# Performance work log

Hardware: AMD Instinct MI355X
Metric: run time of the kernel (lower is better)

Reference implementation:

```python
import jax, jax.numpy as jnp
import numpy as np

L = 4096      # number of nodes (treated as sequence length, batch=1)
D = 256       # in_channels == out_channels
H = 8         # heads
DH = D // H   # head dim = 32
NUM_EDGE_TYPES = 14


def setup_inputs() -> dict:
    key = jax.random.key(0)
    ks = jax.random.split(key, 7)
    x = jax.random.normal(ks[0], (L, D), dtype=jnp.float32)
    mask = jax.random.randint(ks[1], (L, L), 0, NUM_EDGE_TYPES, dtype=jnp.int64)
    s = 1.0 / np.sqrt(D)
    in_proj_w = jax.random.uniform(ks[2], (3 * D, D), jnp.float32, -s, s)
    in_proj_b = jnp.zeros((3 * D,), jnp.float32)
    out_proj_w = jax.random.uniform(ks[3], (D, D), jnp.float32, -s, s)
    out_proj_b = jnp.zeros((D,), jnp.float32)
    edge_bias = jax.random.normal(ks[4], (NUM_EDGE_TYPES, H), dtype=jnp.float32) * 0.02
    return {"x": x, "mask": mask, "in_proj_w": in_proj_w, "in_proj_b": in_proj_b,
            "out_proj_w": out_proj_w, "out_proj_b": out_proj_b, "edge_bias": edge_bias}


def reference(x, mask, in_proj_w, in_proj_b, out_proj_w, out_proj_b, edge_bias):
    # x: (L, D) node features -> viewed as batch-1 self-attention, edge-aware scores.
    qkv = x @ in_proj_w.T + in_proj_b                 # (L, 3D)
    q, k, v = jnp.split(qkv, 3, axis=-1)              # each (L, D)
    q = q.reshape(L, H, DH).transpose(1, 0, 2)        # (H, L, DH)
    k = k.reshape(L, H, DH).transpose(1, 0, 2)
    v = v.reshape(L, H, DH).transpose(1, 0, 2)
    scale = 1.0 / jnp.sqrt(jnp.asarray(DH, x.dtype))
    scores = jnp.einsum('hqd,hkd->hqk', q, k) * scale  # (H, L, L)
    # edge-type bias folded into attention scores: lookup (L,L)->(L,L,H)->(H,L,L)
    scores = scores + edge_bias[mask].transpose(2, 0, 1)
    attn = jax.nn.softmax(scores, axis=-1)             # (H, L, L)
    out = jnp.einsum('hqk,hkd->hqd', attn, v)          # (H, L, DH)
    out = out.transpose(1, 0, 2).reshape(L, D)         # merge heads
    return out @ out_proj_w.T + out_proj_b             # (L, D)
```

## Files before the change

kernel.cpp:

```cpp
#include <hip/hip_runtime.h>
#include <hip/hip_bf16.h>
#include <string.h>

#define L 4096
#define D 256
#define H 8
#define DH 32

typedef __attribute__((ext_vector_type(8))) short bf16x8;
typedef __attribute__((ext_vector_type(4))) float f32x4;

#define LOG2E 1.4426950408889634f
#define RS (0.17677669529663688f * LOG2E)

__device__ __forceinline__ ushort f2bf(float f) {
    union { float f; unsigned int i; } v; v.f = f;
    unsigned int x = v.i;
    return (ushort)((x + 0x7fffu + ((x >> 16) & 1u)) >> 16);
}
__device__ __forceinline__ bf16x8 cvt8(const float* p) {
    float4 a = *(const float4*)p;
    float4 b = *(const float4*)(p + 4);
    bf16x8 r;
    r[0] = (short)f2bf(a.x); r[1] = (short)f2bf(a.y);
    r[2] = (short)f2bf(a.z); r[3] = (short)f2bf(a.w);
    r[4] = (short)f2bf(b.x); r[5] = (short)f2bf(b.y);
    r[6] = (short)f2bf(b.z); r[7] = (short)f2bf(b.w);
    return r;
}
__device__ __forceinline__ unsigned int pkbf(float a, float b) {
    float2 t; t.x = a; t.y = b;
    __hip_bfloat162 r = __float22bfloat162_rn(t);
    unsigned int u; memcpy(&u, &r, 4);
    return u;
}
__device__ __forceinline__ float uaf(unsigned int u) {
    union { unsigned int u; float f; } v; v.u = u; return v.f;
}

__device__ __forceinline__ int ksig(int u) {
    return 32 * (u >> 5) + 16 * ((u >> 2) & 1) + 4 * ((u >> 3) & 3) + (u & 3);
}

__global__ __launch_bounds__(256) void pack_kernel(
        const int* __restrict__ mask, const float* __restrict__ x,
        const float* __restrict__ wi, const float* __restrict__ wo,
        unsigned int* __restrict__ m2, ushort* __restrict__ xb,
        ushort* __restrict__ wib, ushort* __restrict__ wob)
{
    const int b = blockIdx.x;
    const int tid = threadIdx.x;
    if (b < 512) {
        __shared__ unsigned int rb[8 * 1025];
        const int4* src = (const int4*)(mask + (size_t)b * 8 * 4096);
#pragma unroll
        for (int i = 0; i < 32; i++) {
            const int g = i * 256 + tid;
            int4 v = src[g];
            rb[(g >> 10) * 1025 + (g & 1023)] =
                ((unsigned int)(v.x & 15) << 4)  | ((unsigned int)(v.y & 15) << 12) |
                ((unsigned int)(v.z & 15) << 20) | ((unsigned int)(v.w & 15) << 28);
        }
        __syncthreads();
        const int t = b >> 1, half = b & 1;
#pragma unroll
        for (int i = 0; i < 32; i++) {
            const int dd = i * 256 + tid;
            const int nt = dd & 3, s = (dd >> 2) & 7, qd = (dd >> 5) & 3, kt = dd >> 7;
            const unsigned int w =
                rb[s * 1025 + kt * 16 + 8 * (nt >> 1) + 2 * qd + (nt & 1)];
            const unsigned int e0 = (w >> 4) & 15u, e1 = (w >> 12) & 15u;
            const unsigned int e2 = (w >> 20) & 15u, e3 = w >> 28;
            const unsigned int p01 = e0 * 14u + e1, p23 = e2 * 14u + e3;
            m2[(size_t)t * 16384 + kt * 256 + (qd * 16 + 8 * half + s) * 4 + nt] =
                (p01 * 68u) | ((p23 * 68u) << 16);
        }
    } else if (b < 1024) {
        const int t = (b - 512) * 256 + tid;
        ((bf16x8*)xb)[t] = cvt8(x + t * 8);
    } else if (b < 1120) {
        const int t = (b - 1024) * 256 + tid;
        ((bf16x8*)wib)[t] = cvt8(wi + t * 8);
    } else {
        const int t = (b - 1120) * 256 + tid;
        ((bf16x8*)wob)[t] = cvt8(wo + t * 8);
    }
}

__global__ __launch_bounds__(256) void qkv_kernel(
        const ushort* __restrict__ xb, const ushort* __restrict__ wb,
        const float* __restrict__ b,
        ushort* __restrict__ Qb, ushort* __restrict__ Kb, ushort* __restrict__ Vt)
{
    const int lane = threadIdx.x & 63, wv = threadIdx.x >> 6;
    const int quad = lane >> 4, l15 = lane & 15;
    const int m0 = blockIdx.x * 64 + wv * 16;
    const int n0 = blockIdx.y * 64;

    f32x4 acc[4] = {};
    for (int ks = 0; ks < 8; ks++) {
        const int kd = ks * 32 + quad * 8;
        bf16x8 af = *(const bf16x8*)(xb + (m0 + l15) * D + kd);
#pragma unroll
        for (int nt = 0; nt < 4; nt++) {
            bf16x8 bfr = *(const bf16x8*)(wb + (n0 + nt * 16 + l15) * D + kd);
            acc[nt] = __builtin_amdgcn_mfma_f32_16x16x32_bf16(af, bfr, acc[nt], 0, 0, 0);
        }
    }
#pragma unroll
    for (int nt = 0; nt < 4; nt++) {
        const int j = n0 + nt * 16 + l15;
        const float bias = b[j];
#pragma unroll
        for (int r = 0; r < 4; r++) {
            const int row = m0 + quad * 4 + r;
            const float val = acc[nt][r] + bias;
            if (j < 256) {
                Qb[((j >> 5) * L + row) * DH + (j & 31)] = f2bf(val * RS);
            } else if (j < 512) {
                const int jj = j - 256;
                const int srow = (row & ~63) + ksig(row & 63);
                Kb[((jj >> 5) * L + srow) * DH + (jj & 31)] = f2bf(val);
            } else {
                const int jj = j - 512;
                Vt[((jj >> 5) * DH + (jj & 31)) * L + row] = f2bf(val);
            }
        }
    }
}

__global__ __launch_bounds__(512) void attn_kernel(
        const ushort* __restrict__ Qb, const ushort* __restrict__ Kb,
        const ushort* __restrict__ Vt, const unsigned char* __restrict__ m2,
        const float* __restrict__ edge_bias, ushort* __restrict__ Ob)
{
    __shared__ unsigned int lutp[196 * 17];
    __shared__ float red[7 * 576];

    const int tid = threadIdx.x;
    const int lane = tid & 63, wv = tid >> 6;
    const int quad = lane >> 4, l15 = lane & 15;

    const int bid = blockIdx.x;
    const int xr = bid & 7, j = bid >> 3;
    const int qg = xr * 16 + (j >> 3);
    const int h  = j & 7;
    const int q0 = qg * 32;
    const int kt0 = wv * 8;

    for (int p = tid; p < 196; p += 512) {
        const int e1 = (p * 2341) >> 15;
        const int e2 = p - 14 * e1;
        const unsigned int v = pkbf(edge_bias[e1 * H + h] * LOG2E,
                                    edge_bias[e2 * H + h] * LOG2E);
#pragma unroll
        for (int c = 0; c < 17; c++) lutp[p * 17 + c] = v;
    }
    __syncthreads();

    const bf16x8 qfA = *(const bf16x8*)(Qb + (h * L + q0 + l15) * DH + quad * 8);
    const bf16x8 qfB = *(const bf16x8*)(Qb + (h * L + q0 + 16 + l15) * DH + quad * 8);
    const char* lutb = (const char*)lutp + l15 * 4;

    const ushort* Kl = Kb + h * L * DH + kt0 * 64 * DH + l15 * DH + quad * 8;
    const ushort* Va = Vt + (h * DH + l15) * L + kt0 * 64 + quad * 8;
    const ushort* Vb = Vt + (h * DH + 16 + l15) * L + kt0 * 64 + quad * 8;
    const unsigned char* mpA = m2 + (size_t)(2 * qg) * 65536
                             + (size_t)kt0 * 1024 + lane * 16;
    const unsigned char* mpB = mpA + 65536;

    f32x4 o0A = {}, o1A = {}, osA = {};
    f32x4 o0B = {}, o1B = {}, osB = {};
    bf16x8 ones;
#pragma unroll
    for (int i = 0; i < 8; i++) ones[i] = (short)0x3F80;

    for (int kt = 0; kt < 8; kt++) {
        const int4 mA4 = *(const int4*)(mpA + kt * 1024);
        const int4 mB4 = *(const int4*)(mpB + kt * 1024);
        const unsigned int mA[4] = {(unsigned int)mA4.x, (unsigned int)mA4.y,
                                    (unsigned int)mA4.z, (unsigned int)mA4.w};
        const unsigned int mB[4] = {(unsigned int)mB4.x, (unsigned int)mB4.y,
                                    (unsigned int)mB4.z, (unsigned int)mB4.w};

#pragma unroll
        for (int half = 0; half < 2; half++) {
            union { bf16x8 v; unsigned int u[4]; } pfA, pfB;
#pragma unroll
            for (int nt2 = 0; nt2 < 2; nt2++) {
                const int nt = half * 2 + nt2;
                bf16x8 kf = *(const bf16x8*)(Kl + (kt * 64 + nt * 16) * DH);
                f32x4 z = {};
                f32x4 svA = __builtin_amdgcn_mfma_f32_16x16x32_bf16(kf, qfA, z, 0, 0, 0);
                f32x4 svB = __builtin_amdgcn_mfma_f32_16x16x32_bf16(kf, qfB, z, 0, 0, 0);
                const unsigned int wA = mA[nt], wB = mB[nt];
                const unsigned int dA0 = *(const unsigned int*)(lutb + (wA & 0xFFFFu));
                const unsigned int dA1 = *(const unsigned int*)(lutb + (wA >> 16));
                const unsigned int dB0 = *(const unsigned int*)(lutb + (wB & 0xFFFFu));
                const unsigned int dB1 = *(const unsigned int*)(lutb + (wB >> 16));
                float a0 = __builtin_amdgcn_exp2f(svA[0] + uaf(dA0 << 16));
                float a1 = __builtin_amdgcn_exp2f(svA[1] + uaf(dA0 & 0xFFFF0000u));
                float a2 = __builtin_amdgcn_exp2f(svA[2] + uaf(dA1 << 16));
                float a3 = __builtin_amdgcn_exp2f(svA[3] + uaf(dA1 & 0xFFFF0000u));
                float b0 = __builtin_amdgcn_exp2f(svB[0] + uaf(dB0 << 16));
                float b1 = __builtin_amdgcn_exp2f(svB[1] + uaf(dB0 & 0xFFFF0000u));
                float b2 = __builtin_amdgcn_exp2f(svB[2] + uaf(dB1 << 16));
                float b3 = __builtin_amdgcn_exp2f(svB[3] + uaf(dB1 & 0xFFFF0000u));
                pfA.u[nt2 * 2]     = pkbf(a0, a1);
                pfA.u[nt2 * 2 + 1] = pkbf(a2, a3);
                pfB.u[nt2 * 2]     = pkbf(b0, b1);
                pfB.u[nt2 * 2 + 1] = pkbf(b2, b3);
            }
            bf16x8 va = *(const bf16x8*)(Va + kt * 64 + half * 32);
            bf16x8 vb = *(const bf16x8*)(Vb + kt * 64 + half * 32);
            __builtin_amdgcn_s_setprio(1);
            o0A = __builtin_amdgcn_mfma_f32_16x16x32_bf16(va,   pfA.v, o0A, 0, 0, 0);
            o1A = __builtin_amdgcn_mfma_f32_16x16x32_bf16(vb,   pfA.v, o1A, 0, 0, 0);
            osA = __builtin_amdgcn_mfma_f32_16x16x32_bf16(ones, pfA.v, osA, 0, 0, 0);
            o0B = __builtin_amdgcn_mfma_f32_16x16x32_bf16(va,   pfB.v, o0B, 0, 0, 0);
            o1B = __builtin_amdgcn_mfma_f32_16x16x32_bf16(vb,   pfB.v, o1B, 0, 0, 0);
            osB = __builtin_amdgcn_mfma_f32_16x16x32_bf16(ones, pfB.v, osB, 0, 0, 0);
            __builtin_amdgcn_s_setprio(0);
        }
    }

    if (wv > 0) {
        float* s = red + (wv - 1) * 576;
        *(f32x4*)(s +       lane * 4) = o0A;
        *(f32x4*)(s + 256 + lane * 4) = o1A;
        s[512 + lane] = osA[0];
    }
    __syncthreads();
    if (wv == 0) {
#pragma unroll
        for (int sl = 0; sl < 7; sl++) {
            const float* s = red + sl * 576;
            o0A += *(const f32x4*)(s +       lane * 4);
            o1A += *(const f32x4*)(s + 256 + lane * 4);
            osA[0] += s[512 + lane];
        }
        const float invA = 1.f / osA[0];
        ushort* orA = Ob + (size_t)(q0 + l15) * D + h * 32;
        uint2 u;
        u.x = pkbf(o0A[0] * invA, o0A[1] * invA);
        u.y = pkbf(o0A[2] * invA, o0A[3] * invA);
        *(uint2*)(orA + quad * 4) = u;
        u.x = pkbf(o1A[0] * invA, o1A[1] * invA);
        u.y = pkbf(o1A[2] * invA, o1A[3] * invA);
        *(uint2*)(orA + 16 + quad * 4) = u;
    }
    __syncthreads();
    if (wv > 0) {
        float* s = red + (wv - 1) * 576;
        *(f32x4*)(s +       lane * 4) = o0B;
        *(f32x4*)(s + 256 + lane * 4) = o1B;
        s[512 + lane] = osB[0];
    }
    __syncthreads();
    if (wv == 0) {
#pragma unroll
        for (int sl = 0; sl < 7; sl++) {
            const float* s = red + sl * 576;
            o0B += *(const f32x4*)(s +       lane * 4);
            o1B += *(const f32x4*)(s + 256 + lane * 4);
            osB[0] += s[512 + lane];
        }
        const float invB = 1.f / osB[0];
        ushort* orB = Ob + (size_t)(q0 + 16 + l15) * D + h * 32;
        uint2 u;
        u.x = pkbf(o0B[0] * invB, o0B[1] * invB);
        u.y = pkbf(o0B[2] * invB, o0B[3] * invB);
        *(uint2*)(orB + quad * 4) = u;
        u.x = pkbf(o1B[0] * invB, o1B[1] * invB);
        u.y = pkbf(o1B[2] * invB, o1B[3] * invB);
        *(uint2*)(orB + 16 + quad * 4) = u;
    }
}

__global__ __launch_bounds__(256) void oproj_kernel(
        const ushort* __restrict__ Ob, const ushort* __restrict__ wb,
        const float* __restrict__ b, float* __restrict__ out)
{
    const int lane = threadIdx.x & 63, wv = threadIdx.x >> 6;
    const int quad = lane >> 4, l15 = lane & 15;
    const int m0 = blockIdx.x * 64 + wv * 16;
    const int n0 = blockIdx.y * 64;

    f32x4 acc[4] = {};
    for (int ks = 0; ks < 8; ks++) {
        const int kd = ks * 32 + quad * 8;
        bf16x8 af = *(const bf16x8*)(Ob + (m0 + l15) * D + kd);
#pragma unroll
        for (int nt = 0; nt < 4; nt++) {
            bf16x8 bfr = *(const bf16x8*)(wb + (n0 + nt * 16 + l15) * D + kd);
            acc[nt] = __builtin_amdgcn_mfma_f32_16x16x32_bf16(af, bfr, acc[nt], 0, 0, 0);
        }
    }
#pragma unroll
    for (int nt = 0; nt < 4; nt++) {
        const int j = n0 + nt * 16 + l15;
        const float bias = b[j];
#pragma unroll
        for (int r = 0; r < 4; r++) {
            const int orow = m0 + quad * 4 + r;
            out[orow * D + j] = acc[nt][r] + bias;
        }
    }
}

extern "C" void kernel_launch(void* const* d_in, const int* in_sizes, int n_in,
                              void* d_out, int out_size, void* d_ws, size_t ws_size,
                              hipStream_t stream) {
    const float* x     = (const float*)d_in[0];
    const int*   mask  = (const int*)d_in[1];
    const float* in_w  = (const float*)d_in[2];
    const float* in_b  = (const float*)d_in[3];
    const float* out_w = (const float*)d_in[4];
    const float* out_b = (const float*)d_in[5];
    const float* eb    = (const float*)d_in[6];

    ushort* ws = (ushort*)d_ws;
    ushort* Qb  = ws;
    ushort* Kb  = Qb + H * L * DH;
    ushort* Vt  = Kb + H * L * DH;
    ushort* xb  = Vt + H * L * DH;
    ushort* wib = xb + L * D;
    ushort* wob = wib + 3 * D * D;
    unsigned char* m2 = (unsigned char*)(wob + D * D);
    ushort* Ob = (ushort*)(m2 + (size_t)L * L);
    float* out = (float*)d_out;

    pack_kernel<<<dim3(1152), 256, 0, stream>>>(mask, x, in_w, out_w,
                                                (unsigned int*)m2, xb, wib, wob);
    qkv_kernel<<<dim3(64, 12), 256, 0, stream>>>(xb, wib, in_b, Qb, Kb, Vt);
    attn_kernel<<<dim3(1024), 512, 0, stream>>>(Qb, Kb, Vt, m2, eb, Ob);
    oproj_kernel<<<dim3(64, 4), 256, 0, stream>>>(Ob, wob, out_b, out);
}
```

Baseline: 183.5 us.

## Widen edge-bias LUT replicas, prefetch mask words, shrink reduction LDS, remap block order

The per-head edge-bias lookup table is replicated 32 times with a 128-byte stride instead of 17 times with a 68-byte stride, and the mask-packing kernel is changed to emit matching byte offsets. This targets LDS bank conflicts when lanes index the table. Mask words for the next key tile are now loaded one iteration ahead to hide global latency. The cross-wave reduction buffer is cut from 576 to 320 floats per wave by reducing o0 and o1 in separate passes, which adds more barriers but lowers LDS use, possibly raising occupancy. Blocks are also remapped so heads vary fastest, which changes L2 locality.

```diff
diff --git a/kernel.cpp b/kernel.cpp
--- a/kernel.cpp
+++ b/kernel.cpp
@@ -73,7 +73,7 @@
             const unsigned int e2 = (w >> 20) & 15u, e3 = w >> 28;
             const unsigned int p01 = e0 * 14u + e1, p23 = e2 * 14u + e3;
             m2[(size_t)t * 16384 + kt * 256 + (qd * 16 + 8 * half + s) * 4 + nt] =
-                (p01 * 68u) | ((p23 * 68u) << 16);
+                (p01 * 128u) | ((p23 * 128u) << 16);
         }
     } else if (b < 1024) {
         const int t = (b - 512) * 256 + tid;
@@ -134,33 +134,31 @@
         const ushort* __restrict__ Vt, const unsigned char* __restrict__ m2,
         const float* __restrict__ edge_bias, ushort* __restrict__ Ob)
 {
-    __shared__ unsigned int lutp[196 * 17];
-    __shared__ float red[7 * 576];
+    __shared__ unsigned int lutp[196 * 32];
+    __shared__ float red[7 * 320];
 
     const int tid = threadIdx.x;
     const int lane = tid & 63, wv = tid >> 6;
     const int quad = lane >> 4, l15 = lane & 15;
 
     const int bid = blockIdx.x;
-    const int xr = bid & 7, j = bid >> 3;
-    const int qg = xr * 16 + (j >> 3);
-    const int h  = j & 7;
+    const int h  = bid & 7;
+    const int qg = bid >> 3;
     const int q0 = qg * 32;
     const int kt0 = wv * 8;
 
-    for (int p = tid; p < 196; p += 512) {
+    for (int i = tid; i < 196 * 32; i += 512) {
+        const int p = i >> 5;
         const int e1 = (p * 2341) >> 15;
         const int e2 = p - 14 * e1;
-        const unsigned int v = pkbf(edge_bias[e1 * H + h] * LOG2E,
-                                    edge_bias[e2 * H + h] * LOG2E);
-#pragma unroll
-        for (int c = 0; c < 17; c++) lutp[p * 17 + c] = v;
+        lutp[i] = pkbf(edge_bias[e1 * H + h] * LOG2E,
+                       edge_bias[e2 * H + h] * LOG2E);
     }
     __syncthreads();
 
     const bf16x8 qfA = *(const bf16x8*)(Qb + (h * L + q0 + l15) * DH + quad * 8);
     const bf16x8 qfB = *(const bf16x8*)(Qb + (h * L + q0 + 16 + l15) * DH + quad * 8);
-    const char* lutb = (const char*)lutp + l15 * 4;
+    const char* lutb = (const char*)lutp + (lane & 31) * 4;
 
     const ushort* Kl = Kb + h * L * DH + kt0 * 64 * DH + l15 * DH + quad * 8;
     const ushort* Va = Vt + (h * DH + l15) * L + kt0 * 64 + quad * 8;
@@ -175,9 +173,13 @@
 #pragma unroll
     for (int i = 0; i < 8; i++) ones[i] = (short)0x3F80;
 
+    int4 mA4 = *(const int4*)(mpA);
+    int4 mB4 = *(const int4*)(mpB);
+
     for (int kt = 0; kt < 8; kt++) {
-        const int4 mA4 = *(const int4*)(mpA + kt * 1024);
-        const int4 mB4 = *(const int4*)(mpB + kt * 1024);
+        const int nk = (kt + 1) & 7;
+        const int4 nA4 = *(const int4*)(mpA + nk * 1024);
+        const int4 nB4 = *(const int4*)(mpB + nk * 1024);
         const unsigned int mA[4] = {(unsigned int)mA4.x, (unsigned int)mA4.y,
                                     (unsigned int)mA4.z, (unsigned int)mA4.w};
         const unsigned int mB[4] = {(unsigned int)mB4.x, (unsigned int)mB4.y,
@@ -222,55 +224,74 @@
             osB = __builtin_amdgcn_mfma_f32_16x16x32_bf16(ones, pfB.v, osB, 0, 0, 0);
             __builtin_amdgcn_s_setprio(0);
         }
-    }
-
+        mA4 = nA4; mB4 = nB4;
+    }
+
+    float invA, invB;
+    ushort* orA = Ob + (size_t)(q0 + l15) * D + h * 32;
+    ushort* orB = Ob + (size_t)(q0 + 16 + l15) * D + h * 32;
+    uint2 u;
     if (wv > 0) {
-        float* s = red + (wv - 1) * 576;
-        *(f32x4*)(s +       lane * 4) = o0A;
-        *(f32x4*)(s + 256 + lane * 4) = o1A;
-        s[512 + lane] = osA[0];
+        float* s = red + (wv - 1) * 320;
+        *(f32x4*)(s + lane * 4) = o0A;
+        s[256 + lane] = osA[0];
     }
     __syncthreads();
     if (wv == 0) {
 #pragma unroll
         for (int sl = 0; sl < 7; sl++) {
-            const float* s = red + sl * 576;
-            o0A += *(const f32x4*)(s +       lane * 4);
-            o1A += *(const f32x4*)(s + 256 + lane * 4);
-            osA[0] += s[512 + lane];
-        }
-        const float invA = 1.f / osA[0];
-        ushort* orA = Ob + (size_t)(q0 + l15) * D + h * 32;
-        uint2 u;
+            const float* s = red + sl * 320;
+            o0A += *(const f32x4*)(s + lane * 4);
+            osA[0] += s[256 + lane];
+        }
+        invA = 1.f / osA[0];
         u.x = pkbf(o0A[0] * invA, o0A[1] * invA);
         u.y = pkbf(o0A[2] * invA, o0A[3] * invA);
         *(uint2*)(orA + quad * 4) = u;
+    }
+    __syncthreads();
+    if (wv > 0) {
+        float* s = red + (wv - 1) * 320;
+        *(f32x4*)(s + lane * 4) = o1A;
+    }
+    __syncthreads();
+    if (wv == 0) {
+#pragma unroll
+        for (int sl = 0; sl < 7; sl++)
+            o1A += *(const f32x4*)(red + sl * 320 + lane * 4);
         u.x = pkbf(o1A[0] * invA, o1A[1] * invA);
         u.y = pkbf(o1A[2] * invA, o1A[3] * invA);
         *(uint2*)(orA + 16 + quad * 4) = u;
     }
     __syncthreads();
     if (wv > 0) {
-        float* s = red + (wv - 1) * 576;
-        *(f32x4*)(s +       lane * 4) = o0B;
-        *(f32x4*)(s + 256 + lane * 4) = o1B;
-        s[512 + lane] = osB[0];
+        float* s = red + (wv - 1) * 320;
+        *(f32x4*)(s + lane * 4) = o0B;
+        s[256 + lane] = osB[0];
     }
     __syncthreads();
     if (wv == 0) {
 #pragma unroll
         for (int sl = 0; sl < 7; sl++) {
-            const float* s = red + sl * 576;
-            o0B += *(const f32x4*)(s +       lane * 4);
-            o1B += *(const f32x4*)(s + 256 + lane * 4);
-            osB[0] += s[512 + lane];
-        }
-        const float invB = 1.f / osB[0];
-        ushort* orB = Ob + (size_t)(q0 + 16 + l15) * D + h * 32;
-        uint2 u;
+            const float* s = red + sl * 320;
+            o0B += *(const f32x4*)(s + lane * 4);
+            osB[0] += s[256 + lane];
+        }
+        invB = 1.f / osB[0];
         u.x = pkbf(o0B[0] * invB, o0B[1] * invB);
         u.y = pkbf(o0B[2] * invB, o0B[3] * invB);
         *(uint2*)(orB + quad * 4) = u;
+    }
+    __syncthreads();
+    if (wv > 0) {
+        float* s = red + (wv - 1) * 320;
+        *(f32x4*)(s + lane * 4) = o1B;
+    }
+    __syncthreads();
+    if (wv == 0) {
+#pragma unroll
+        for (int sl = 0; sl < 7; sl++)
+            o1B += *(const f32x4*)(red + sl * 320 + lane * 4);
         u.x = pkbf(o1B[0] * invB, o1B[1] * invB);
         u.y = pkbf(o1B[2] * invB, o1B[3] * invB);
         *(uint2*)(orB + 16 + quad * 4) = u;
```

After: 189.0 us. 1.03x slower.

## Store bf16 operands in MFMA fragment-tiled layout for coalesced GEMM loads

Applied to the files above, without the earlier changes.

The pack kernel now writes x, in_proj_w and out_proj_w as bf16 in a 16-row by 8-element fragment-tiled layout. The attention kernel writes its output O in the same layout. The QKV and output-projection GEMMs then read their operand fragments as contiguous 16-byte chunks per lane instead of strided rows, which should improve load coalescing. The attention output stores become more scattered in exchange, and the layouts must agree across the three kernels.

```diff
diff --git a/kernel.cpp b/kernel.cpp
--- a/kernel.cpp
+++ b/kernel.cpp
@@ -41,6 +41,7 @@
 __device__ __forceinline__ int ksig(int u) {
     return 32 * (u >> 5) + 16 * ((u >> 2) & 1) + 4 * ((u >> 3) & 3) + (u & 3);
 }
+
 
 __global__ __launch_bounds__(256) void pack_kernel(
         const int* __restrict__ mask, const float* __restrict__ x,
@@ -76,14 +77,17 @@
                 (p01 * 68u) | ((p23 * 68u) << 16);
         }
     } else if (b < 1024) {
-        const int t = (b - 512) * 256 + tid;
-        ((bf16x8*)xb)[t] = cvt8(x + t * 8);
+        const int g = (b - 512) * 256 + tid;
+        const int l = g & 15, kd = (g >> 4) & 31, mg = g >> 9;
+        ((bf16x8*)xb)[g] = cvt8(x + (mg * 16 + l) * 256 + kd * 8);
     } else if (b < 1120) {
-        const int t = (b - 1024) * 256 + tid;
-        ((bf16x8*)wib)[t] = cvt8(wi + t * 8);
+        const int g = (b - 1024) * 256 + tid;
+        const int l = g & 15, kd = (g >> 4) & 31, mg = g >> 9;
+        ((bf16x8*)wib)[g] = cvt8(wi + (mg * 16 + l) * 256 + kd * 8);
     } else {
-        const int t = (b - 1120) * 256 + tid;
-        ((bf16x8*)wob)[t] = cvt8(wo + t * 8);
+        const int g = (b - 1120) * 256 + tid;
+        const int l = g & 15, kd = (g >> 4) & 31, mg = g >> 9;
+        ((bf16x8*)wob)[g] = cvt8(wo + (mg * 16 + l) * 256 + kd * 8);
     }
 }
 
@@ -96,14 +100,16 @@
     const int quad = lane >> 4, l15 = lane & 15;
     const int m0 = blockIdx.x * 64 + wv * 16;
     const int n0 = blockIdx.y * 64;
+    const ushort* ap = xb + (size_t)(blockIdx.x * 4 + wv) * 4096 + l15 * 8;
+    const ushort* bp = wb + (size_t)(blockIdx.y * 4) * 4096 + l15 * 8;
 
     f32x4 acc[4] = {};
     for (int ks = 0; ks < 8; ks++) {
-        const int kd = ks * 32 + quad * 8;
-        bf16x8 af = *(const bf16x8*)(xb + (m0 + l15) * D + kd);
+        const int kdi = (ks * 4 + quad) * 128;
+        bf16x8 af = *(const bf16x8*)(ap + kdi);
 #pragma unroll
         for (int nt = 0; nt < 4; nt++) {
-            bf16x8 bfr = *(const bf16x8*)(wb + (n0 + nt * 16 + l15) * D + kd);
+            bf16x8 bfr = *(const bf16x8*)(bp + nt * 4096 + kdi);
             acc[nt] = __builtin_amdgcn_mfma_f32_16x16x32_bf16(af, bfr, acc[nt], 0, 0, 0);
         }
     }
@@ -224,6 +230,12 @@
         }
     }
 
+    ushort* obase = Ob + (size_t)(2 * qg) * 4096 + l15 * 8 + (quad & 1) * 4;
+    ushort* or0A = obase + (h * 4 + (quad >> 1)) * 128;
+    ushort* or1A = obase + (h * 4 + 2 + (quad >> 1)) * 128;
+    ushort* or0B = or0A + 4096;
+    ushort* or1B = or1A + 4096;
+
     if (wv > 0) {
         float* s = red + (wv - 1) * 576;
         *(f32x4*)(s +       lane * 4) = o0A;
@@ -240,14 +252,13 @@
             osA[0] += s[512 + lane];
         }
         const float invA = 1.f / osA[0];
-        ushort* orA = Ob + (size_t)(q0 + l15) * D + h * 32;
         uint2 u;
         u.x = pkbf(o0A[0] * invA, o0A[1] * invA);
         u.y = pkbf(o0A[2] * invA, o0A[3] * invA);
-        *(uint2*)(orA + quad * 4) = u;
+        *(uint2*)or0A = u;
         u.x = pkbf(o1A[0] * invA, o1A[1] * invA);
         u.y = pkbf(o1A[2] * invA, o1A[3] * invA);
-        *(uint2*)(orA + 16 + quad * 4) = u;
+        *(uint2*)or1A = u;
     }
     __syncthreads();
     if (wv > 0) {
@@ -266,14 +277,13 @@
             osB[0] += s[512 + lane];
         }
         const float invB = 1.f / osB[0];
-        ushort* orB = Ob + (size_t)(q0 + 16 + l15) * D + h * 32;
         uint2 u;
         u.x = pkbf(o0B[0] * invB, o0B[1] * invB);
         u.y = pkbf(o0B[2] * invB, o0B[3] * invB);
-        *(uint2*)(orB + quad * 4) = u;
+        *(uint2*)or0B = u;
         u.x = pkbf(o1B[0] * invB, o1B[1] * invB);
         u.y = pkbf(o1B[2] * invB, o1B[3] * invB);
-        *(uint2*)(orB + 16 + quad * 4) = u;
+        *(uint2*)or1B = u;
     }
 }
 
@@ -285,14 +295,16 @@
     const int quad = lane >> 4, l15 = lane & 15;
     const int m0 = blockIdx.x * 64 + wv * 16;
     const int n0 = blockIdx.y * 64;
+    const ushort* ap = Ob + (size_t)(blockIdx.x * 4 + wv) * 4096 + l15 * 8;
+    const ushort* bp = wb + (size_t)(blockIdx.y * 4) * 4096 + l15 * 8;
 
     f32x4 acc[4] = {};
     for (int ks = 0; ks < 8; ks++) {
-        const int kd = ks * 32 + quad * 8;
-        bf16x8 af = *(const bf16x8*)(Ob + (m0 + l15) * D + kd);
+        const int kdi = (ks * 4 + quad) * 128;
+        bf16x8 af = *(const bf16x8*)(ap + kdi);
 #pragma unroll
         for (int nt = 0; nt < 4; nt++) {
-            bf16x8 bfr = *(const bf16x8*)(wb + (n0 + nt * 16 + l15) * D + kd);
+            bf16x8 bfr = *(const bf16x8*)(bp + nt * 4096 + kdi);
             acc[nt] = __builtin_amdgcn_mfma_f32_16x16x32_bf16(af, bfr, acc[nt], 0, 0, 0);
         }
     }
```

New measurement: 172.3 us. 6.1% less time.
